# Kernel optimization log

Hardware: AMD Instinct MI355X
Metric: run time of the kernel (lower is better)

## Reference

```python
import jax, jax.numpy as jnp
import numpy as np

EMBED = 1024
HEADS = 16
HD = EMBED // HEADS
FF = 4096
EPS = 1e-5

def _layernorm(x, g, b):
    mu = jnp.mean(x, axis=-1, keepdims=True)
    var = jnp.mean(jnp.square(x - mu), axis=-1, keepdims=True)
    return (x - mu) * jax.lax.rsqrt(var + EPS) * g + b

def setup_inputs() -> dict:
    key = jax.random.key(0)
    ks = jax.random.split(key, 10)
    s = 0.02
    return {
        "x": jax.random.normal(ks[0], (4, 2048, EMBED), dtype=jnp.float32),
        "Wq": jax.random.normal(ks[1], (EMBED, EMBED), dtype=jnp.float32) * s,
        "Wk": jax.random.normal(ks[2], (EMBED, EMBED), dtype=jnp.float32) * s,
        "Wv": jax.random.normal(ks[3], (EMBED, EMBED), dtype=jnp.float32) * s,
        "Wo": jax.random.normal(ks[4], (EMBED, EMBED), dtype=jnp.float32) * s,
        "bo": jnp.zeros((EMBED,), dtype=jnp.float32),
        "W1": jax.random.normal(ks[5], (EMBED, FF), dtype=jnp.float32) * s,
        "b1": jnp.zeros((FF,), dtype=jnp.float32),
        "W2": jax.random.normal(ks[6], (FF, EMBED), dtype=jnp.float32) * s,
        "b2": jnp.zeros((EMBED,), dtype=jnp.float32),
        "g1": jnp.ones((EMBED,), dtype=jnp.float32),
        "be1": jnp.zeros((EMBED,), dtype=jnp.float32),
        "g2": jnp.ones((EMBED,), dtype=jnp.float32),
        "be2": jnp.zeros((EMBED,), dtype=jnp.float32),
    }

def reference(x, Wq, Wk, Wv, Wo, bo, W1, b1, W2, b2, g1, be1, g2, be2):
    B, T, _ = x.shape
    # --- pre-norm self-attention (dropout = identity in eval) ---
    h = _layernorm(x, g1, be1)
    q = (h @ Wq).reshape(B, T, HEADS, HD).transpose(0, 2, 1, 3)  # bhtd
    k = (h @ Wk).reshape(B, T, HEADS, HD).transpose(0, 2, 1, 3)
    v = (h @ Wv).reshape(B, T, HEADS, HD).transpose(0, 2, 1, 3)
    scores = jnp.einsum('bhid,bhjd->bhij', q, k) / jnp.sqrt(jnp.float32(HD))
    causal = jnp.tril(jnp.ones((T, T), dtype=bool))
    scores = jnp.where(causal[None, None], scores, -jnp.inf)
    attn = jax.nn.softmax(scores, axis=-1)
    out = jnp.einsum('bhij,bhjd->bhid', attn, v)
    out = out.transpose(0, 2, 1, 3).reshape(B, T, EMBED)
    out = out @ Wo + bo
    x = x + out
    # --- pre-norm GELU FFN ---
    h2 = _layernorm(x, g2, be2)
    ff = jax.nn.gelu(h2 @ W1 + b1, approximate=False) @ W2 + b2
    return x + ff
```

## Files before the change

kernel.cpp:

```cpp
#include <hip/hip_runtime.h>

typedef unsigned short u16;
typedef __attribute__((ext_vector_type(8))) short bf16x8;
typedef __attribute__((ext_vector_type(4))) float f32x4;

#define EMBED 1024
#define FFDIM 4096
#define SEQ   2048
#define NTOK  8192
#define ATT_C 0.18033688011112042f

__device__ __forceinline__ u16 f2bf(float f) {
  union { float f; unsigned int u; } c; c.f = f;
  unsigned int r = ((c.u >> 16) & 1u) + 0x7fffu;
  return (u16)((c.u + r) >> 16);
}

__device__ __forceinline__ unsigned cvtpk(float lo, float hi) {
  unsigned r;
  asm("v_cvt_pk_bf16_f32 %0, %1, %2" : "=v"(r) : "v"(lo), "v"(hi));
  return r;
}

__device__ __forceinline__ void gload16(const u16* g, u16* l) {
  __builtin_amdgcn_global_load_lds((const __attribute__((address_space(1))) void*)g,
                                   (__attribute__((address_space(3))) void*)l, 16, 0, 0);
}

__global__ __launch_bounds__(256) void wtrans(const float* __restrict__ W,
                                              u16* __restrict__ Wt, int K, int N) {
  __shared__ float tile[32][33];
  const int tx = threadIdx.x & 31, ty = threadIdx.x >> 5;
  const int n0 = blockIdx.x << 5, k0 = blockIdx.y << 5;
#pragma unroll
  for (int r = 0; r < 32; r += 8)
    tile[ty + r][tx] = W[(size_t)(k0 + ty + r) * N + n0 + tx];
  __syncthreads();
#pragma unroll
  for (int r = 0; r < 32; r += 8)
    Wt[(size_t)(n0 + ty + r) * K + k0 + tx] = f2bf(tile[tx][ty + r]);
}

__global__ __launch_bounds__(256) void vtrans(const u16* __restrict__ qkv,
                                              u16* __restrict__ Vt) {
  __shared__ u16 tile[32][33];
  const int tx = threadIdx.x & 31, ty = threadIdx.x >> 5;
  const int t0 = blockIdx.x << 5;
  const int rg0 = blockIdx.y << 5;
  const int bh = rg0 >> 6, d0 = rg0 & 63;
  const int b = bh >> 4, h = bh & 15;
#pragma unroll
  for (int r = 0; r < 32; r += 8)
    tile[ty + r][tx] = qkv[(size_t)(b * SEQ + t0 + ty + r) * 3072 + 2048 + h * 64 + d0 + tx];
  __syncthreads();
#pragma unroll
  for (int r = 0; r < 32; r += 8)
    Vt[(size_t)(rg0 + ty + r) * SEQ + t0 + tx] = tile[tx][ty + r];
}

__global__ __launch_bounds__(256) void ln_kernel(const float* __restrict__ xin,
                                                 const float* __restrict__ gamma,
                                                 const float* __restrict__ beta,
                                                 u16* __restrict__ out) {
  const int row = blockIdx.x, tid = threadIdx.x;
  const float4 v = reinterpret_cast<const float4*>(xin + (size_t)row * EMBED)[tid];
  float s  = v.x + v.y + v.z + v.w;
  float ss = v.x * v.x + v.y * v.y + v.z * v.z + v.w * v.w;
#pragma unroll
  for (int m = 1; m < 64; m <<= 1) { s += __shfl_xor(s, m); ss += __shfl_xor(ss, m); }
  __shared__ float red[8];
  if ((tid & 63) == 0) { red[tid >> 6] = s; red[4 + (tid >> 6)] = ss; }
  __syncthreads();
  s  = red[0] + red[1] + red[2] + red[3];
  ss = red[4] + red[5] + red[6] + red[7];
  const float mean = s * (1.0f / EMBED);
  const float var  = ss * (1.0f / EMBED) - mean * mean;
  const float rstd = rsqrtf(var + 1e-5f);
  const float4 g  = reinterpret_cast<const float4*>(gamma)[tid];
  const float4 bb = reinterpret_cast<const float4*>(beta)[tid];
  ushort4 o;
  o.x = f2bf((v.x - mean) * rstd * g.x + bb.x);
  o.y = f2bf((v.y - mean) * rstd * g.y + bb.y);
  o.z = f2bf((v.z - mean) * rstd * g.z + bb.z);
  o.w = f2bf((v.w - mean) * rstd * g.w + bb.w);
  reinterpret_cast<ushort4*>(out + (size_t)row * EMBED)[tid] = o;
}

template <int NREP, int EPI>
__global__ __launch_bounds__(512, 2) void gemm2(const u16* __restrict__ A,
                                                const u16* __restrict__ Bt,
                                                void* __restrict__ Cv,
                                                const float* __restrict__ bias,
                                                const float* __restrict__ res,
                                                int M, int N, int K) {
  constexpr int BN = NREP * 64;
  constexpr int TLOADS = 4 + NREP;
  __shared__ __align__(16) u16 As[2][256 * 64];
  __shared__ __align__(16) u16 Bs[2][BN * 64];

  const int tid = threadIdx.x;
  const int lane = tid & 63, wid = tid >> 6;
  const int l4 = lane >> 4, l15 = lane & 15;
  const int wm = wid >> 2, wn = wid & 3;

  const int gx = gridDim.x;
  const int nwg = gx * (int)gridDim.y;
  const int flat = (int)blockIdx.y * gx + (int)blockIdx.x;
  const int cpx = nwg >> 3;
  const int swz = (flat & 7) * cpx + (flat >> 3);
  const int brow = (swz / gx) << 8;
  const int bcol = (swz % gx) * BN;

  const f32x4 z4 = {0.f, 0.f, 0.f, 0.f};
  f32x4 acc[8][NREP];
#pragma unroll
  for (int m = 0; m < 8; ++m)
#pragma unroll
    for (int n = 0; n < NREP; ++n) acc[m][n] = z4;

  const int srow = tid >> 3;
  const int scolb = ((tid & 7) << 4) ^ ((srow & 7) << 4);
  const u16* gA = A  + (size_t)(brow + srow) * K + (scolb >> 1);
  const u16* gB = Bt + (size_t)(bcol + srow) * K + (scolb >> 1);
  const int lbase = wid * 64 * 8;

  const int nk = K >> 6;

#define STAGE(c, kt)                                                            \
  do {                                                                          \
    const u16* a_ = gA + (size_t)(kt) * 64;                                     \
    const u16* b_ = gB + (size_t)(kt) * 64;                                     \
    _Pragma("unroll")                                                           \
    for (int k_ = 0; k_ < 4; ++k_)                                              \
      gload16(a_ + (size_t)k_ * 64 * K, &As[c][lbase + k_ * 512 * 8]);          \
    _Pragma("unroll")                                                           \
    for (int k_ = 0; k_ < NREP; ++k_)                                           \
      gload16(b_ + (size_t)k_ * 64 * K, &Bs[c][lbase + k_ * 512 * 8]);          \
  } while (0)

  STAGE(0, 0);
  STAGE(1, 1);
  asm volatile("s_waitcnt vmcnt(%0)" :: "i"(TLOADS) : "memory");
  __builtin_amdgcn_sched_barrier(0);
  __builtin_amdgcn_s_barrier();
  __builtin_amdgcn_sched_barrier(0);

  const int arow = wm * 128 + l15;
  const int bcl  = wn * (BN / 4) + l15;
  const int kk0  = l4 << 3;
  const int aswz = (arow & 7) << 3;
  const int bswz = (bcl & 7) << 3;

  for (int t = 0; t < nk; ++t) {
    const int c = t & 1;
    const u16* as = As[c];
    const u16* bs = Bs[c];
    bf16x8 af[8], bf[NREP];

#pragma unroll
    for (int m = 0; m < 8; ++m)
      af[m] = *(const bf16x8*)&as[(arow + m * 16) * 64 + (kk0 ^ aswz)];
#pragma unroll
    for (int n = 0; n < NREP; ++n)
      bf[n] = *(const bf16x8*)&bs[(bcl + n * 16) * 64 + (kk0 ^ bswz)];
    __builtin_amdgcn_s_setprio(1);
#pragma unroll
    for (int m = 0; m < 8; ++m)
#pragma unroll
      for (int n = 0; n < NREP; ++n)
        acc[m][n] = __builtin_amdgcn_mfma_f32_16x16x32_bf16(af[m], bf[n], acc[m][n], 0, 0, 0);
    __builtin_amdgcn_s_setprio(0);

#pragma unroll
    for (int m = 0; m < 8; ++m)
      af[m] = *(const bf16x8*)&as[(arow + m * 16) * 64 + ((kk0 + 32) ^ aswz)];
#pragma unroll
    for (int n = 0; n < NREP; ++n)
      bf[n] = *(const bf16x8*)&bs[(bcl + n * 16) * 64 + ((kk0 + 32) ^ bswz)];
    asm volatile("s_waitcnt lgkmcnt(0)" ::: "memory");
    __builtin_amdgcn_sched_barrier(0);
    __builtin_amdgcn_s_barrier();
    __builtin_amdgcn_sched_barrier(0);

    if (t + 2 < nk) STAGE(c, t + 2);

    __builtin_amdgcn_s_setprio(1);
#pragma unroll
    for (int m = 0; m < 8; ++m)
#pragma unroll
      for (int n = 0; n < NREP; ++n)
        acc[m][n] = __builtin_amdgcn_mfma_f32_16x16x32_bf16(af[m], bf[n], acc[m][n], 0, 0, 0);
    __builtin_amdgcn_s_setprio(0);

    if (t + 2 < nk) {
      asm volatile("s_waitcnt vmcnt(%0)" :: "i"(TLOADS) : "memory");
    } else {
      asm volatile("s_waitcnt vmcnt(0)" ::: "memory");
    }
    __builtin_amdgcn_sched_barrier(0);
    __builtin_amdgcn_s_barrier();
    __builtin_amdgcn_sched_barrier(0);
  }
#undef STAGE

  const int rowb = brow + wm * 128 + (l4 << 2);
  const int colb = bcol + wn * (BN / 4) + l15;
#pragma unroll
  for (int n = 0; n < NREP; ++n) {
    const int col = colb + n * 16;
    float bv = 0.f;
    if (EPI != 0) bv = bias[col];
#pragma unroll
    for (int m = 0; m < 8; ++m) {
#pragma unroll
      for (int j = 0; j < 4; ++j) {
        const int row = rowb + m * 16 + j;
        const float v = acc[m][n][j];
        if (EPI == 0) {
          ((u16*)Cv)[(size_t)row * N + col] = f2bf(v);
        } else if (EPI == 1) {
          ((float*)Cv)[(size_t)row * N + col] = v + bv + res[(size_t)row * N + col];
        } else {
          const float t2 = v + bv;
          const float gl = 0.5f * t2 * (1.0f + erff(t2 * 0.70710678118654752f));
          ((u16*)Cv)[(size_t)row * N + col] = f2bf(gl);
        }
      }
    }
  }
}

__global__ __launch_bounds__(512) void attn_fwd(const u16* __restrict__ qkv,
                                                const u16* __restrict__ Vt,
                                                u16* __restrict__ attn) {
  __shared__ __align__(16) u16 Ks[64 * 72];
  __shared__ __align__(16) u16 Vs[64 * 72];
  __shared__ __align__(16) u16 Ps[8 * 16 * 72];
  const int tid = threadIdx.x, lane = tid & 63, wid = tid >> 6;
  const int l4 = lane >> 4, l15 = lane & 15;
  const int bh = blockIdx.y, b = bh >> 4, h = bh & 15;
  const size_t bt0 = (size_t)b * SEQ;
  u16* Pw = &Ps[wid * 16 * 72];

  const int sr = tid >> 3;
  const int sc0 = (tid & 7) << 3;
  const u16* kbase = qkv + bt0 * 3072 + 1024 + h * 64;
  const u16* vbase = Vt + (size_t)bh * 64 * SEQ;
  const f32x4 z4 = {0.f, 0.f, 0.f, 0.f};

#pragma unroll
  for (int ph = 0; ph < 2; ++ph) {
    const int Qb = ((ph == 0) ? (int)blockIdx.x : 15 - (int)blockIdx.x) << 7;
    const int qw = Qb + wid * 16;
    const int qlane = qw + l15;

    const u16* qp = qkv + (bt0 + qlane) * 3072 + h * 64 + (l4 << 3);
    const bf16x8 aq0 = *(const bf16x8*)qp;
    const bf16x8 aq1 = *(const bf16x8*)(qp + 32);

    f32x4 o[4];
#pragma unroll
    for (int dt = 0; dt < 4; ++dt) o[dt] = z4;
    float mrun = -1e30f, lrun = 0.f;

    bf16x8 kp = *(const bf16x8*)(kbase + (size_t)sr * 3072 + sc0);
    bf16x8 vp = *(const bf16x8*)(vbase + (size_t)sr * SEQ + sc0);

    const int jend = Qb + 128;
    for (int j0 = 0; j0 < jend; j0 += 64) {
      __syncthreads();
      *(bf16x8*)&Ks[sr * 72 + sc0] = kp;
      *(bf16x8*)&Vs[sr * 72 + sc0] = vp;
      __syncthreads();

      if (j0 + 64 < jend) {
        kp = *(const bf16x8*)(kbase + (size_t)(j0 + 64 + sr) * 3072 + sc0);
        vp = *(const bf16x8*)(vbase + (size_t)sr * SEQ + j0 + 64 + sc0);
      }

      if (j0 > qw + 15) continue;
      const int nt = min(4, ((qw + 15 - j0) >> 4) + 1);

      f32x4 s[4];
#pragma unroll
      for (int t = 0; t < 4; ++t) {
        if (t < nt) {
          const bf16x8 ak0 = *(const bf16x8*)&Ks[(t * 16 + l15) * 72 + (l4 << 3)];
          const bf16x8 ak1 = *(const bf16x8*)&Ks[(t * 16 + l15) * 72 + 32 + (l4 << 3)];
          f32x4 a = z4;
          a = __builtin_amdgcn_mfma_f32_16x16x32_bf16(ak0, aq0, a, 0, 0, 0);
          a = __builtin_amdgcn_mfma_f32_16x16x32_bf16(ak1, aq1, a, 0, 0, 0);
          s[t] = a;
        }
      }

      float mt = -1e30f;
#pragma unroll
      for (int t = 0; t < 4; ++t) {
        if (t < nt) {
          if (j0 + t * 16 + 15 > qw) {
            const int kvb = j0 + t * 16 + (l4 << 2);
#pragma unroll
            for (int j = 0; j < 4; ++j)
              if (kvb + j > qlane) s[t][j] = -1e30f;
          }
          mt = fmaxf(mt, fmaxf(fmaxf(s[t][0], s[t][1]), fmaxf(s[t][2], s[t][3])));
        }
      }
      mt = fmaxf(mt, __shfl_xor(mt, 16));
      mt = fmaxf(mt, __shfl_xor(mt, 32));

      const bool skip = __all(mt <= mrun + 44.0f);
      float scq = 1.0f;
      if (!skip) {
        const float mn = fmaxf(mrun, mt);
        scq = exp2f((mrun - mn) * ATT_C);
        mrun = mn;
      }
      const float mc = mrun * ATT_C;

      float ls = 0.f;
      uint2 pw[4];
#pragma unroll
      for (int t = 0; t < 4; ++t) {
        if (t < nt) {
          const float p0 = exp2f(__builtin_fmaf(s[t][0], ATT_C, -mc));
          const float p1 = exp2f(__builtin_fmaf(s[t][1], ATT_C, -mc));
          const float p2 = exp2f(__builtin_fmaf(s[t][2], ATT_C, -mc));
          const float p3 = exp2f(__builtin_fmaf(s[t][3], ATT_C, -mc));
          ls += (p0 + p1) + (p2 + p3);
          pw[t].x = cvtpk(p0, p1);
          pw[t].y = cvtpk(p2, p3);
        } else {
          pw[t].x = 0u; pw[t].y = 0u;
        }
      }
#pragma unroll
      for (int t = 0; t < 4; ++t)
        *(uint2*)&Pw[l15 * 72 + t * 16 + (l4 << 2)] = pw[t];

      ls += __shfl_xor(ls, 16);
      ls += __shfl_xor(ls, 32);

      if (!skip) {
        lrun = lrun * scq + ls;
#pragma unroll
        for (int dt = 0; dt < 4; ++dt)
#pragma unroll
          for (int j = 0; j < 4; ++j) o[dt][j] *= scq;
      } else {
        lrun += ls;
      }

      const int nc = (nt + 1) >> 1;
#pragma unroll
      for (int c = 0; c < 2; ++c) {
        if (c < nc) {
          const bf16x8 ap = *(const bf16x8*)&Pw[l15 * 72 + c * 32 + (l4 << 3)];
#pragma unroll
          for (int dt = 0; dt < 4; ++dt) {
            const bf16x8 bv = *(const bf16x8*)&Vs[(dt * 16 + l15) * 72 + c * 32 + (l4 << 3)];
            o[dt] = __builtin_amdgcn_mfma_f32_16x16x32_bf16(bv, ap, o[dt], 0, 0, 0);
          }
        }
      }
    }

    const float rl = 1.0f / lrun;
#pragma unroll
    for (int dt = 0; dt < 4; ++dt) {
      uint2 w;
      w.x = cvtpk(o[dt][0] * rl, o[dt][1] * rl);
      w.y = cvtpk(o[dt][2] * rl, o[dt][3] * rl);
      *(uint2*)&Pw[l15 * 72 + dt * 16 + (l4 << 2)] = w;
    }
#pragma unroll
    for (int rep = 0; rep < 2; ++rep) {
      const int unit = rep * 64 + lane;
      const int r = unit >> 3, c = unit & 7;
      const bf16x8 v = *(const bf16x8*)&Pw[r * 72 + c * 8];
      *(bf16x8*)&attn[(bt0 + qw + r) * EMBED + h * 64 + c * 8] = v;
    }
  }
}

extern "C" void kernel_launch(void* const* d_in, const int* in_sizes, int n_in,
                              void* d_out, int out_size, void* d_ws, size_t ws_size,
                              hipStream_t stream) {
  const float* x   = (const float*)d_in[0];
  const float* Wq  = (const float*)d_in[1];
  const float* Wk  = (const float*)d_in[2];
  const float* Wv  = (const float*)d_in[3];
  const float* Wo  = (const float*)d_in[4];
  const float* bo  = (const float*)d_in[5];
  const float* W1  = (const float*)d_in[6];
  const float* b1  = (const float*)d_in[7];
  const float* W2  = (const float*)d_in[8];
  const float* b2  = (const float*)d_in[9];
  const float* g1  = (const float*)d_in[10];
  const float* be1 = (const float*)d_in[11];
  const float* g2  = (const float*)d_in[12];
  const float* be2 = (const float*)d_in[13];

  char* ws = (char*)d_ws;
  u16* wqkv_t = (u16*)(ws + 0);
  u16* wo_t   = (u16*)(ws + 6291456);
  u16* w1_t   = (u16*)(ws + 8388608);
  u16* w2_t   = (u16*)(ws + 16777216);
  u16* hbuf   = (u16*)(ws + 25165824);
  u16* qkv    = (u16*)(ws + 41943040);
  u16* ff1    = (u16*)(ws + 41943040);
  u16* vt     = (u16*)(ws + 92274688);
  u16* attnb  = (u16*)(ws + 109051904);
  float* x2   = (float*)(ws + 125829120);
  float* outp = (float*)d_out;

  dim3 blk(256);
  wtrans<<<dim3(32, 32),  blk, 0, stream>>>(Wq, wqkv_t,               1024, 1024);
  wtrans<<<dim3(32, 32),  blk, 0, stream>>>(Wk, wqkv_t + 1024 * 1024, 1024, 1024);
  wtrans<<<dim3(32, 32),  blk, 0, stream>>>(Wv, wqkv_t + 2048 * 1024, 1024, 1024);
  wtrans<<<dim3(32, 32),  blk, 0, stream>>>(Wo, wo_t,                 1024, 1024);
  wtrans<<<dim3(128, 32), blk, 0, stream>>>(W1, w1_t,                 1024, 4096);
  wtrans<<<dim3(32, 128), blk, 0, stream>>>(W2, w2_t,                 4096, 1024);

  ln_kernel<<<dim3(8192), blk, 0, stream>>>(x, g1, be1, hbuf);
  gemm2<4, 0><<<dim3(12, 32), dim3(512), 0, stream>>>(hbuf, wqkv_t, qkv, nullptr, nullptr,
                                                      8192, 3072, 1024);
  vtrans<<<dim3(64, 128), blk, 0, stream>>>(qkv, vt);
  attn_fwd<<<dim3(8, 64), dim3(512), 0, stream>>>(qkv, vt, attnb);
  gemm2<2, 1><<<dim3(8, 32), dim3(512), 0, stream>>>(attnb, wo_t, x2, bo, x,
                                                     8192, 1024, 1024);
  ln_kernel<<<dim3(8192), blk, 0, stream>>>(x2, g2, be2, hbuf);
  gemm2<4, 2><<<dim3(16, 32), dim3(512), 0, stream>>>(hbuf, w1_t, ff1, b1, nullptr,
                                                      8192, 4096, 1024);
  gemm2<2, 1><<<dim3(8, 32), dim3(512), 0, stream>>>(ff1, w2_t, outp, b2, x2,
                                                     8192, 1024, 4096);
}
```

Before: 418.2 us.

## Restructure GEMM main loop into four-phase interleaved load/MFMA pipeline

Replaces the GEMM K-loop with a finer-grained schedule. Global-to-LDS loads are split into half-tile pieces for A and B and issued in four phases per K-step, each phase pairing one LDS fragment read with half of the MFMA work, so memory traffic overlaps compute more evenly. Launch bounds drop to one workgroup per SIMD pair so more registers are available for the double fragment buffers, and the QKV projection switches to a narrower 128-column tile with twice as many blocks. The cost is more barriers per iteration and possibly lower occupancy.

```diff
diff --git a/kernel.cpp b/kernel.cpp
--- a/kernel.cpp
+++ b/kernel.cpp
@@ -87,14 +87,14 @@
 }
 
 template <int NREP, int EPI>
-__global__ __launch_bounds__(512, 2) void gemm2(const u16* __restrict__ A,
+__global__ __launch_bounds__(512, 1) void gemm3(const u16* __restrict__ A,
                                                 const u16* __restrict__ Bt,
                                                 void* __restrict__ Cv,
                                                 const float* __restrict__ bias,
                                                 const float* __restrict__ res,
                                                 int M, int N, int K) {
   constexpr int BN = NREP * 64;
-  constexpr int TLOADS = 4 + NREP;
+  constexpr int VMC = (NREP == 4) ? 6 : 4;
   __shared__ __align__(16) u16 As[2][256 * 64];
   __shared__ __align__(16) u16 Bs[2][BN * 64];
 
@@ -120,30 +120,42 @@
 
   const int srow = tid >> 3;
   const int scolb = ((tid & 7) << 4) ^ ((srow & 7) << 4);
-  const u16* gA = A  + (size_t)(brow + srow) * K + (scolb >> 1);
-  const u16* gB = Bt + (size_t)(bcol + srow) * K + (scolb >> 1);
-  const int lbase = wid * 64 * 8;
+  const u16* gAs = A  + (size_t)(brow + srow) * K + (scolb >> 1);
+  const u16* gBs = Bt + (size_t)(bcol + srow) * K + (scolb >> 1);
+  const int lA = wid * 512;
 
   const int nk = K >> 6;
 
-#define STAGE(c, kt)                                                            \
+#define STAGE_A(c, t, h)                                                        \
   do {                                                                          \
-    const u16* a_ = gA + (size_t)(kt) * 64;                                     \
-    const u16* b_ = gB + (size_t)(kt) * 64;                                     \
-    _Pragma("unroll")                                                           \
-    for (int k_ = 0; k_ < 4; ++k_)                                              \
-      gload16(a_ + (size_t)k_ * 64 * K, &As[c][lbase + k_ * 512 * 8]);          \
-    _Pragma("unroll")                                                           \
-    for (int k_ = 0; k_ < NREP; ++k_)                                           \
-      gload16(b_ + (size_t)k_ * 64 * K, &Bs[c][lbase + k_ * 512 * 8]);          \
+    gload16(gAs + (size_t)((h) * 128) * K + (size_t)(t) * 64,                   \
+            &As[c][(h) * 8192 + lA]);                                           \
+    gload16(gAs + (size_t)((h) * 128 + 64) * K + (size_t)(t) * 64,              \
+            &As[c][(h) * 8192 + 4096 + lA]);                                    \
   } while (0)
-
-  STAGE(0, 0);
-  STAGE(1, 1);
-  asm volatile("s_waitcnt vmcnt(%0)" :: "i"(TLOADS) : "memory");
-  __builtin_amdgcn_sched_barrier(0);
-  __builtin_amdgcn_s_barrier();
-  __builtin_amdgcn_sched_barrier(0);
+#define STAGE_B(c, t, h)                                                        \
+  do {                                                                          \
+    if constexpr (NREP == 4) {                                                  \
+      gload16(gBs + (size_t)((h) * 128) * K + (size_t)(t) * 64,                 \
+              &Bs[c][(h) * 8192 + lA]);                                         \
+      gload16(gBs + (size_t)((h) * 128 + 64) * K + (size_t)(t) * 64,            \
+              &Bs[c][(h) * 8192 + 4096 + lA]);                                  \
+    } else {                                                                    \
+      gload16(gBs + (size_t)((h) * 64) * K + (size_t)(t) * 64,                  \
+              &Bs[c][(h) * 4096 + lA]);                                         \
+    }                                                                           \
+  } while (0)
+
+#define GATE                                                                    \
+  asm volatile("s_waitcnt vmcnt(%0)" :: "i"(VMC) : "memory");                   \
+  __builtin_amdgcn_sched_barrier(0);                                            \
+  __builtin_amdgcn_s_barrier();                                                 \
+  asm volatile("s_waitcnt lgkmcnt(0)" ::: "memory");                            \
+  __builtin_amdgcn_sched_barrier(0)
+#define ENDBAR                                                                  \
+  __builtin_amdgcn_sched_barrier(0);                                            \
+  __builtin_amdgcn_s_barrier();                                                 \
+  __builtin_amdgcn_sched_barrier(0)
 
   const int arow = wm * 128 + l15;
   const int bcl  = wn * (BN / 4) + l15;
@@ -151,57 +163,68 @@
   const int aswz = (arow & 7) << 3;
   const int bswz = (bcl & 7) << 3;
 
+#define READ_A(dst, c, ks)                                                      \
+  _Pragma("unroll")                                                             \
+  for (int m = 0; m < 8; ++m)                                                   \
+    dst[m] = *(const bf16x8*)&As[c][(arow + m * 16) * 64 + ((kk0 + (ks) * 32) ^ aswz)];
+#define READ_B(dst, c, ks)                                                      \
+  _Pragma("unroll")                                                             \
+  for (int n = 0; n < NREP; ++n)                                                \
+    dst[n] = *(const bf16x8*)&Bs[c][(bcl + n * 16) * 64 + ((kk0 + (ks) * 32) ^ bswz)];
+#define MFMA_H(MH, AF, BF)                                                      \
+  __builtin_amdgcn_s_setprio(1);                                                \
+  _Pragma("unroll")                                                             \
+  for (int m = 0; m < 4; ++m)                                                   \
+    _Pragma("unroll")                                                           \
+    for (int n = 0; n < NREP; ++n)                                              \
+      acc[(MH) * 4 + m][n] = __builtin_amdgcn_mfma_f32_16x16x32_bf16(           \
+          AF[(MH) * 4 + m], BF[n], acc[(MH) * 4 + m][n], 0, 0, 0);              \
+  __builtin_amdgcn_s_setprio(0)
+
+  STAGE_A(0, 0, 0);
+  STAGE_A(0, 0, 1);
+  STAGE_B(0, 0, 0);
+  STAGE_B(0, 0, 1);
+  if (nk > 1) STAGE_A(1, 1, 0);
+  asm volatile("s_waitcnt vmcnt(%0)" :: "i"(VMC) : "memory");
+  __builtin_amdgcn_sched_barrier(0);
+  __builtin_amdgcn_s_barrier();
+  __builtin_amdgcn_sched_barrier(0);
+
+  bf16x8 afk0[8], afk1[8], bfk0[NREP], bfk1[NREP];
+
   for (int t = 0; t < nk; ++t) {
-    const int c = t & 1;
-    const u16* as = As[c];
-    const u16* bs = Bs[c];
-    bf16x8 af[8], bf[NREP];
-
-#pragma unroll
-    for (int m = 0; m < 8; ++m)
-      af[m] = *(const bf16x8*)&as[(arow + m * 16) * 64 + (kk0 ^ aswz)];
-#pragma unroll
-    for (int n = 0; n < NREP; ++n)
-      bf[n] = *(const bf16x8*)&bs[(bcl + n * 16) * 64 + (kk0 ^ bswz)];
-    __builtin_amdgcn_s_setprio(1);
-#pragma unroll
-    for (int m = 0; m < 8; ++m)
-#pragma unroll
-      for (int n = 0; n < NREP; ++n)
-        acc[m][n] = __builtin_amdgcn_mfma_f32_16x16x32_bf16(af[m], bf[n], acc[m][n], 0, 0, 0);
-    __builtin_amdgcn_s_setprio(0);
-
-#pragma unroll
-    for (int m = 0; m < 8; ++m)
-      af[m] = *(const bf16x8*)&as[(arow + m * 16) * 64 + ((kk0 + 32) ^ aswz)];
-#pragma unroll
-    for (int n = 0; n < NREP; ++n)
-      bf[n] = *(const bf16x8*)&bs[(bcl + n * 16) * 64 + ((kk0 + 32) ^ bswz)];
-    asm volatile("s_waitcnt lgkmcnt(0)" ::: "memory");
-    __builtin_amdgcn_sched_barrier(0);
-    __builtin_amdgcn_s_barrier();
-    __builtin_amdgcn_sched_barrier(0);
-
-    if (t + 2 < nk) STAGE(c, t + 2);
-
-    __builtin_amdgcn_s_setprio(1);
-#pragma unroll
-    for (int m = 0; m < 8; ++m)
-#pragma unroll
-      for (int n = 0; n < NREP; ++n)
-        acc[m][n] = __builtin_amdgcn_mfma_f32_16x16x32_bf16(af[m], bf[n], acc[m][n], 0, 0, 0);
-    __builtin_amdgcn_s_setprio(0);
-
-    if (t + 2 < nk) {
-      asm volatile("s_waitcnt vmcnt(%0)" :: "i"(TLOADS) : "memory");
-    } else {
-      asm volatile("s_waitcnt vmcnt(0)" ::: "memory");
-    }
-    __builtin_amdgcn_sched_barrier(0);
-    __builtin_amdgcn_s_barrier();
-    __builtin_amdgcn_sched_barrier(0);
+    const int c = t & 1, cn = c ^ 1;
+    READ_A(afk0, c, 0);
+    if (t + 1 < nk) STAGE_A(cn, t + 1, 1);
+    GATE;
+    if (t > 0) { MFMA_H(1, afk1, bfk1); }
+    ENDBAR;
+    READ_B(bfk0, c, 0);
+    if (t + 1 < nk) STAGE_B(cn, t + 1, 0);
+    GATE;
+    MFMA_H(0, afk0, bfk0);
+    ENDBAR;
+    READ_A(afk1, c, 1);
+    if (t + 1 < nk) STAGE_B(cn, t + 1, 1);
+    GATE;
+    MFMA_H(1, afk0, bfk0);
+    ENDBAR;
+    READ_B(bfk1, c, 1);
+    if (t + 2 < nk) STAGE_A(c, t + 2, 0);
+    GATE;
+    MFMA_H(0, afk1, bfk1);
+    ENDBAR;
   }
-#undef STAGE
+  MFMA_H(1, afk1, bfk1);
+
+#undef STAGE_A
+#undef STAGE_B
+#undef GATE
+#undef ENDBAR
+#undef READ_A
+#undef READ_B
+#undef MFMA_H
 
   const int rowb = brow + wm * 128 + (l4 << 2);
   const int colb = bcol + wn * (BN / 4) + l15;
@@ -424,15 +447,15 @@
   wtrans<<<dim3(32, 128), blk, 0, stream>>>(W2, w2_t,                 4096, 1024);
 
   ln_kernel<<<dim3(8192), blk, 0, stream>>>(x, g1, be1, hbuf);
-  gemm2<4, 0><<<dim3(12, 32), dim3(512), 0, stream>>>(hbuf, wqkv_t, qkv, nullptr, nullptr,
+  gemm3<2, 0><<<dim3(24, 32), dim3(512), 0, stream>>>(hbuf, wqkv_t, qkv, nullptr, nullptr,
                                                       8192, 3072, 1024);
   vtrans<<<dim3(64, 128), blk, 0, stream>>>(qkv, vt);
   attn_fwd<<<dim3(8, 64), dim3(512), 0, stream>>>(qkv, vt, attnb);
-  gemm2<2, 1><<<dim3(8, 32), dim3(512), 0, stream>>>(attnb, wo_t, x2, bo, x,
+  gemm3<2, 1><<<dim3(8, 32), dim3(512), 0, stream>>>(attnb, wo_t, x2, bo, x,
                                                      8192, 1024, 1024);
   ln_kernel<<<dim3(8192), blk, 0, stream>>>(x2, g2, be2, hbuf);
-  gemm2<4, 2><<<dim3(16, 32), dim3(512), 0, stream>>>(hbuf, w1_t, ff1, b1, nullptr,
+  gemm3<4, 2><<<dim3(16, 32), dim3(512), 0, stream>>>(hbuf, w1_t, ff1, b1, nullptr,
                                                       8192, 4096, 1024);
-  gemm2<2, 1><<<dim3(8, 32), dim3(512), 0, stream>>>(ff1, w2_t, outp, b2, x2,
+  gemm3<2, 1><<<dim3(8, 32), dim3(512), 0, stream>>>(ff1, w2_t, outp, b2, x2,
                                                      8192, 1024, 4096);
 }
```

Result: slower. 446.4 us (+6.7%).
